# Optimization experiments

Hardware: AMD Instinct MI355X
Metric: run time of the kernel (lower is better)

Reference implementation:

```python
import jax, jax.numpy as jnp
import numpy as np

NEG = -1.0e30  # log-space 'zero' that is safe in fp32
EPS = 1e-7     # keras.backend.ctc_batch_cost epsilon


def setup_inputs() -> dict:
    key = jax.random.key(0)
    k1, k2 = jax.random.split(key)
    B, T, C, L = 256, 512, 256, 128
    # y_pred are post-softmax probabilities, as expected by ctc_batch_cost
    logits = jax.random.normal(k1, (B, T, C), dtype=jnp.float32)
    y_pred = jax.nn.softmax(logits, axis=-1)
    # labels in [0, C-1): never equal to blank index C-1
    y_true = jax.random.randint(k2, (B, L), 0, C - 1, dtype=jnp.int32)
    return {"y_true": y_true, "y_pred": y_pred}


def _ctc_batch_cost(y_true, y_pred):
    """Faithful keras.backend.ctc_batch_cost with full input/label lengths.

    y_true: [B, L] int labels (no blanks). y_pred: [B, T, C] probabilities.
    Blank index = C - 1 (TF v1 ctc_loss convention). Returns [B, 1] loss.
    """
    B, T, C = y_pred.shape
    L = y_true.shape[1]
    blank = C - 1
    S = 2 * L + 1  # extended label: blank, l0, blank, l1, ..., blank

    logp = jnp.log(y_pred + EPS)                                # [B, T, C]
    ext = jnp.full((B, S), blank, dtype=y_true.dtype).at[:, 1::2].set(y_true)
    # per-(t, s) log prob of the extended symbol
    lp = jnp.take_along_axis(logp, ext[:, None, :].astype(jnp.int32), axis=2)  # [B, T, S]

    # skip transition s-2 -> s allowed iff s >= 2, ext[s] != blank, ext[s] != ext[s-2]
    ext_m2 = jnp.pad(ext, ((0, 0), (2, 0)), constant_values=blank)[:, :S]
    skip = (ext != blank) & (ext != ext_m2) & (jnp.arange(S)[None, :] >= 2)

    # alpha init at t=0: only s=0 (blank) and s=1 (first label) reachable
    alpha0 = jnp.where(jnp.arange(S)[None, :] < 2, lp[:, 0, :], NEG)  # [B, S]

    def step(alpha, lp_t):
        p1 = jnp.pad(alpha, ((0, 0), (1, 0)), constant_values=NEG)[:, :S]
        p2 = jnp.pad(alpha, ((0, 0), (2, 0)), constant_values=NEG)[:, :S]
        a = jnp.logaddexp(alpha, p1)
        a = jnp.logaddexp(a, jnp.where(skip, p2, NEG))
        return a + lp_t, None

    lp_time_major = jnp.moveaxis(lp, 1, 0)  # [T, B, S]
    alpha, _ = jax.lax.scan(step, alpha0, lp_time_major[1:])
    # total log-likelihood ends at last blank or last label
    loss = -jnp.logaddexp(alpha[:, S - 1], alpha[:, S - 2])    # [B]
    return loss[:, None]                                        # [B, 1]


def reference(y_true, y_pred):
    # CTCLayer.call computes ctc_batch_cost with input_length = T, label_length = L
    # for every batch row, adds it as a loss, and passes y_pred through. The
    # compute of interest is the loss itself, returned here as [B, 1].
    return _ctc_batch_cost(y_true, y_pred)
```

## Files before the change

### kernel.cpp

```cpp
#include <hip/hip_runtime.h>
#include <math.h>


namespace {
constexpr int Bn = 256;
constexpr int Tn = 512;
constexpr int Cn = 256;
constexpr int Ln = 128;
constexpr int CH = 32;
constexpr int NCHUNK = Tn / CH;
constexpr int SLOTS = 64;
constexpr float EPSf = 1e-7f;
constexpr float LN2f = 0.69314718055994530942f;
constexpr int   TGT  = 100;
}

typedef float f4 __attribute__((ext_vector_type(4)));

#define GLOAD(dst, p) \
    asm volatile("global_load_dwordx4 %0, %1, off" : "=v"(dst) : "v"(p))
#define VMWAIT0() \
    asm volatile("s_waitcnt vmcnt(0)" ::: "memory")

__device__ __forceinline__ float rdl63(float v) {
    return __int_as_float(__builtin_amdgcn_readlane(__float_as_int(v), 63));
}
__device__ __forceinline__ float dpp_shr1(float v) {
    return __int_as_float(__builtin_amdgcn_update_dpp(
        0, __float_as_int(v), 0x138, 0xF, 0xF, true));
}
template <int CTRL>
__device__ __forceinline__ float dpp_max(float m) {
    float o = __int_as_float(__builtin_amdgcn_update_dpp(
        0, __float_as_int(m), CTRL, 0xF, 0xF, true));
    return fmaxf(m, o);
}

__global__ __launch_bounds__(512, 1)
void ctc_fwd(const int* __restrict__ y_true,
             const float* __restrict__ y_pred,
             float* __restrict__ out)
{
    const int b    = blockIdx.x;
    const int tid  = (int)threadIdx.x;
    const int w    = tid >> 6;
    const int lane = tid & 63;

    __shared__ __align__(16) float lds[SLOTS * Cn];

    const f4* gbase = (const f4*)(y_pred + (size_t)b * Tn * Cn);
    f4* ringv = (f4*)lds;

    auto load_chunk = [&](int ch) {
        f4 tmp[5];
        int rows[5];
        #pragma unroll
        for (int k = 0; k < 5; ++k) {
            int rl = (w - 1) + 7 * k;
            rl = rl > CH - 1 ? CH - 1 : rl;
            const int t = ch * CH + rl;
            rows[k] = t;
            GLOAD(tmp[k], gbase + (size_t)t * (Cn / 4) + lane);
        }
        VMWAIT0();
        #pragma unroll
        for (int k = 0; k < 5; ++k)
            ringv[(rows[k] & (SLOTS - 1)) * (Cn / 4) + lane] = tmp[k];
    };

    const int* yt = y_true + b * Ln;
    const int l0 = yt[2 * lane];
    const int l1 = yt[2 * lane + 1];
    const int lm = (lane > 0) ? yt[2 * lane - 1] : -1;
    const float sk1 = (lane > 0 && l0 != lm) ? 1.0f : 0.0f;
    const float sk3 = (l1 != l0) ? 1.0f : 0.0f;

    float a0 = (lane == 0) ? 0x1p100f : 0.0f;
    float a1 = 0.0f, a2 = 0.0f, a3 = 0.0f, a4 = 0.0f;
    int Eacc = -100;

    auto step = [&](float rb, float r0, float r1) {
        const float n = dpp_shr1(a3);
        const float Pb = rb + EPSf;
        const float P0 = r0 + EPSf;
        const float P1 = r1 + EPSf;
        const float na0 = (a0 + n) * Pb;
        const float na1 = fmaf(sk1, n,  a1 + a0) * P0;
        const float na2 = (a2 + a1) * Pb;
        const float na3 = fmaf(sk3, a1, a3 + a2) * P1;
        const float na4 = (a4 + a3) * Pb;
        a0 = na0; a1 = na1; a2 = na2; a3 = na3; a4 = na4;
    };

    auto rescale = [&]() {
        float m = fmaxf(fmaxf(fmaxf(a0, a1), fmaxf(a2, a3)), a4);
        m = dpp_max<0x111>(m);
        m = dpp_max<0x112>(m);
        m = dpp_max<0x114>(m);
        m = dpp_max<0x118>(m);
        m = dpp_max<0x142>(m);
        m = dpp_max<0x143>(m);
        m = rdl63(m);
        int e;
        (void)frexpf(m, &e);
        const int shift = TGT - e;
        a0 = ldexpf(a0, shift);
        a1 = ldexpf(a1, shift);
        a2 = ldexpf(a2, shift);
        a3 = ldexpf(a3, shift);
        a4 = ldexpf(a4, shift);
        Eacc -= shift;
    };

    auto consume_chunk = [&](int c) {
        const int t0 = c * CH;
        int s = (t0 & (SLOTS - 1)) * Cn;
        float rba = lds[s + (Cn - 1)], r0a = lds[s + l0], r1a = lds[s + l1];
        s = ((t0 + 1) & (SLOTS - 1)) * Cn;
        float rbb = lds[s + (Cn - 1)], r0b = lds[s + l0], r1b = lds[s + l1];
        #pragma unroll
        for (int j = 0; j < CH; ++j) {
            float rbn = 0.0f, r0n = 0.0f, r1n = 0.0f;
            if (j < CH - 2) {
                const int ss = ((t0 + j + 2) & (SLOTS - 1)) * Cn;
                rbn = lds[ss + (Cn - 1)];
                r0n = lds[ss + l0];
                r1n = lds[ss + l1];
            }
            step(rba, r0a, r1a);
            rba = rbb; r0a = r0b; r1a = r1b;
            rbb = rbn; r0b = r0n; r1b = r1n;
            if ((j & 15) == 15) rescale();
        }
    };

    if (w > 0) load_chunk(0);
    __syncthreads();
    for (int c = 0; c < NCHUNK; ++c) {
        if (w > 0) {
            if (c + 1 < NCHUNK) load_chunk(c + 1);
        } else {
            consume_chunk(c);
        }
        __syncthreads();
    }

    if (w == 0 && lane == 63) {
        const float sfin = a3 + a4;
        out[b] = -LN2f * (log2f(sfin) + (float)Eacc);
    }
}

extern "C" void kernel_launch(void* const* d_in, const int* in_sizes, int n_in,
                              void* d_out, int out_size, void* d_ws, size_t ws_size,
                              hipStream_t stream) {
    const int*   y_true = (const int*)  d_in[0];
    const float* y_pred = (const float*)d_in[1];
    float* out = (float*)d_out;
    (void)in_sizes; (void)n_in; (void)out_size; (void)d_ws; (void)ws_size;
    ctc_fwd<<<dim3(Bn), dim3(512), 0, stream>>>(y_true, y_pred, out);
}
```

Measured before the change: 195.9 us.

## Stream chunks directly into LDS with deeper async prefetch pipeline

Replaces register-staged global loads with direct global-to-LDS loads, enlarges the LDS ring to 128 time slots and keeps three chunks in flight, using counted vmcnt waits and raw barriers instead of __syncthreads. The consumer wave now prefetches four time steps of LDS reads ahead instead of two. The aim is to hide the single consumer wave's per-chunk wait on global memory latency and remove the register round-trip in the loader waves. The risk is that the raw barrier lacks the LDS fence __syncthreads provides, so visibility depends on the vmcnt accounting being exact. The larger LDS footprint also limits occupancy.

```diff
diff --git a/kernel.cpp b/kernel.cpp
--- a/kernel.cpp
+++ b/kernel.cpp
@@ -1,5 +1,6 @@
 #include <hip/hip_runtime.h>
 #include <math.h>
+#include <stdint.h>
 
 
 namespace {
@@ -9,18 +10,20 @@
 constexpr int Ln = 128;
 constexpr int CH = 32;
 constexpr int NCHUNK = Tn / CH;
-constexpr int SLOTS = 64;
+constexpr int SLOTS = 128;
+constexpr int DEPTH = 3;
 constexpr float EPSf = 1e-7f;
 constexpr float LN2f = 0.69314718055994530942f;
 constexpr int   TGT  = 100;
 }
 
-typedef float f4 __attribute__((ext_vector_type(4)));
+#define VMWAIT(N) asm volatile("s_waitcnt vmcnt(" #N ")" ::: "memory")
 
-#define GLOAD(dst, p) \
-    asm volatile("global_load_dwordx4 %0, %1, off" : "=v"(dst) : "v"(p))
-#define VMWAIT0() \
-    asm volatile("s_waitcnt vmcnt(0)" ::: "memory")
+__device__ __forceinline__ void barrier_raw() {
+    asm volatile("" ::: "memory");
+    __builtin_amdgcn_s_barrier();
+    asm volatile("" ::: "memory");
+}
 
 __device__ __forceinline__ float rdl63(float v) {
     return __int_as_float(__builtin_amdgcn_readlane(__float_as_int(v), 63));
@@ -48,36 +51,36 @@
 
     __shared__ __align__(16) float lds[SLOTS * Cn];
 
-    const f4* gbase = (const f4*)(y_pred + (size_t)b * Tn * Cn);
-    f4* ringv = (f4*)lds;
+    const float* gbase = y_pred + (size_t)b * Tn * Cn;
 
-    auto load_chunk = [&](int ch) {
-        f4 tmp[5];
-        int rows[5];
+    auto issue_chunk = [&](int ch) {
         #pragma unroll
         for (int k = 0; k < 5; ++k) {
             int rl = (w - 1) + 7 * k;
             rl = rl > CH - 1 ? CH - 1 : rl;
             const int t = ch * CH + rl;
-            rows[k] = t;
-            GLOAD(tmp[k], gbase + (size_t)t * (Cn / 4) + lane);
+            const float* gp = gbase + (size_t)t * Cn + lane * 4;
+            float* lp = &lds[(t & (SLOTS - 1)) * Cn];
+            __builtin_amdgcn_global_load_lds(
+                (const __attribute__((address_space(1))) void*)gp,
+                (__attribute__((address_space(3))) void*)lp,
+                16, 0, 0);
         }
-        VMWAIT0();
-        #pragma unroll
-        for (int k = 0; k < 5; ++k)
-            ringv[(rows[k] & (SLOTS - 1)) * (Cn / 4) + lane] = tmp[k];
     };
 
-    const int* yt = y_true + b * Ln;
-    const int l0 = yt[2 * lane];
-    const int l1 = yt[2 * lane + 1];
-    const int lm = (lane > 0) ? yt[2 * lane - 1] : -1;
-    const float sk1 = (lane > 0 && l0 != lm) ? 1.0f : 0.0f;
-    const float sk3 = (l1 != l0) ? 1.0f : 0.0f;
-
-    float a0 = (lane == 0) ? 0x1p100f : 0.0f;
-    float a1 = 0.0f, a2 = 0.0f, a3 = 0.0f, a4 = 0.0f;
+    int l0 = 0, l1 = 0;
+    float sk1 = 0.0f, sk3 = 0.0f;
+    float a0 = 0.0f, a1 = 0.0f, a2 = 0.0f, a3 = 0.0f, a4 = 0.0f;
     int Eacc = -100;
+    if (w == 0) {
+        const int* yt = y_true + b * Ln;
+        l0 = yt[2 * lane];
+        l1 = yt[2 * lane + 1];
+        const int lm = (lane > 0) ? yt[2 * lane - 1] : -1;
+        sk1 = (lane > 0 && l0 != lm) ? 1.0f : 0.0f;
+        sk3 = (l1 != l0) ? 1.0f : 0.0f;
+        a0 = (lane == 0) ? 0x1p100f : 0.0f;
+    }
 
     auto step = [&](float rb, float r0, float r1) {
         const float n = dpp_shr1(a3);
@@ -114,35 +117,52 @@
 
     auto consume_chunk = [&](int c) {
         const int t0 = c * CH;
-        int s = (t0 & (SLOTS - 1)) * Cn;
-        float rba = lds[s + (Cn - 1)], r0a = lds[s + l0], r1a = lds[s + l1];
+        float rb0, r00, r10, rb1, r01, r11;
+        float rb2, r02, r12, rb3, r03, r13;
+        int s = ((t0 + 0) & (SLOTS - 1)) * Cn;
+        rb0 = lds[s + (Cn - 1)]; r00 = lds[s + l0]; r10 = lds[s + l1];
         s = ((t0 + 1) & (SLOTS - 1)) * Cn;
-        float rbb = lds[s + (Cn - 1)], r0b = lds[s + l0], r1b = lds[s + l1];
+        rb1 = lds[s + (Cn - 1)]; r01 = lds[s + l0]; r11 = lds[s + l1];
+        s = ((t0 + 2) & (SLOTS - 1)) * Cn;
+        rb2 = lds[s + (Cn - 1)]; r02 = lds[s + l0]; r12 = lds[s + l1];
+        s = ((t0 + 3) & (SLOTS - 1)) * Cn;
+        rb3 = lds[s + (Cn - 1)]; r03 = lds[s + l0]; r13 = lds[s + l1];
         #pragma unroll
         for (int j = 0; j < CH; ++j) {
             float rbn = 0.0f, r0n = 0.0f, r1n = 0.0f;
-            if (j < CH - 2) {
-                const int ss = ((t0 + j + 2) & (SLOTS - 1)) * Cn;
+            if (j < CH - 4) {
+                const int ss = ((t0 + j + 4) & (SLOTS - 1)) * Cn;
                 rbn = lds[ss + (Cn - 1)];
                 r0n = lds[ss + l0];
                 r1n = lds[ss + l1];
             }
-            step(rba, r0a, r1a);
-            rba = rbb; r0a = r0b; r1a = r1b;
-            rbb = rbn; r0b = r0n; r1b = r1n;
+            step(rb0, r00, r10);
+            rb0 = rb1; r00 = r01; r10 = r11;
+            rb1 = rb2; r01 = r02; r11 = r12;
+            rb2 = rb3; r02 = r03; r12 = r13;
+            rb3 = rbn; r03 = r0n; r13 = r1n;
             if ((j & 15) == 15) rescale();
         }
     };
 
-    if (w > 0) load_chunk(0);
-    __syncthreads();
+    if (w > 0) {
+        issue_chunk(0);
+        issue_chunk(1);
+        issue_chunk(2);
+        VMWAIT(10);
+    }
+    barrier_raw();
+
     for (int c = 0; c < NCHUNK; ++c) {
         if (w > 0) {
-            if (c + 1 < NCHUNK) load_chunk(c + 1);
+            if (c + DEPTH < NCHUNK) issue_chunk(c + DEPTH);
+            if (c <= NCHUNK - 4)      VMWAIT(10);
+            else if (c == NCHUNK - 3) VMWAIT(5);
+            else                      VMWAIT(0);
         } else {
             consume_chunk(c);
         }
-        __syncthreads();
+        barrier_raw();
     }
 
     if (w == 0 && lane == 63) {
```

After: 196.6 us. Within noise of the previous version (+0.4%).
